# Performance work log

Hardware: AMD Instinct MI355X
Metric: run time of the kernel (lower is better)

The kernel has to match this reference:

```python
import math
import jax, jax.numpy as jnp
import numpy as np

B, W, C = 2, 2048, 1024
N, K = 16, 64  # heads, head dim (C // N)


def setup_inputs() -> dict:
    key = jax.random.key(0)
    ks = jax.random.split(key, 6)
    return {
        "in_sequence_bwc": jax.random.normal(ks[0], (B, W, C), dtype=jnp.float32),
        "W_proj": jax.random.normal(ks[1], (C, C), dtype=jnp.float32) * (1.0 / math.sqrt(C)),
        "b_proj": jax.random.normal(ks[2], (C,), dtype=jnp.float32) * 0.01,
        "generators_1nwk": jax.random.normal(ks[3], (1, N, W, K), dtype=jnp.float32),
        "W_mix": jax.random.normal(ks[4], (C, C), dtype=jnp.float32) * (1.0 / math.sqrt(C)),
        "b_mix": jax.random.normal(ks[5], (C,), dtype=jnp.float32) * 0.01,
    }


def reference(in_sequence_bwc, W_proj, b_proj, generators_1nwk, W_mix, b_mix):
    b, w, c = in_sequence_bwc.shape
    # shared projection (torch Linear: x @ W.T + b)
    p_bwc = in_sequence_bwc @ W_proj.T + b_proj
    p_bnwk = p_bwc.reshape(b, w, N, K).transpose(0, 2, 1, 3)  # [b, n, w, k]
    g_nwk = generators_1nwk[0, :, :w, :]  # [n, w, k]
    # data-dependent metric generator: p^T @ G -> [b, n, k, k]
    m_bnkk = jnp.einsum("bnwk,nwl->bnkl", p_bnwk, g_nwk)
    tril_kk = jnp.tril(jnp.ones((K, K), dtype=in_sequence_bwc.dtype))
    m_bnkk = m_bnkk * tril_kk  # lower-triangular mask on k x k
    m_bnkk = m_bnkk @ jnp.swapaxes(m_bnkk, -1, -2)  # PSD metric M M^T
    # bilinear scores: P @ M @ P^T, scaled
    pm_bnwk = jnp.einsum("bnwk,bnkl->bnwl", p_bnwk, m_bnkk)
    scores_bnww = jnp.einsum("bnwk,bnvk->bnwv", pm_bnwk, p_bnwk) / math.sqrt(K)
    causal = jnp.tril(jnp.ones((w, w), dtype=bool))
    scores_bnww = jnp.where(causal, scores_bnww, -jnp.inf)
    attn_bnww = jax.nn.softmax(scores_bnww, axis=-1)
    nudged_bnwk = attn_bnww @ p_bnwk
    nudged_bwc = nudged_bnwk.transpose(0, 2, 1, 3).reshape(b, w, c)
    return nudged_bwc @ W_mix.T + b_mix
```

## Files before the change

kernel.cpp:

```cpp
#include <hip/hip_runtime.h>
#include <math.h>

#define B_  2
#define W_  2048
#define C_  1024
#define NH_ 16
#define KD_ 64

__device__ __forceinline__ int swz2(int r, int c) {
    return (r << 6) + ((((c >> 2) ^ ((r >> 2) & 7)) << 2) | (c & 3));
}
__device__ __forceinline__ void stage_sw2(const float* __restrict__ src,
                                          float* dst, int tid, int nf4) {
    for (int idx = tid; idx < nf4; idx += 256) {
        int r = idx >> 4;
        int c = (idx & 15) << 2;
        *(float4*)&dst[swz2(r, c)] = *(const float4*)(src + (idx << 2));
    }
}

template<int OUT_P_LAYOUT>
__global__ __launch_bounds__(256, 2)
void gemm_nt(const float* __restrict__ A, const float* __restrict__ Bw,
             const float* __restrict__ bias, float* __restrict__ Cout)
{
    __shared__ float As[16][68];
    __shared__ float Bs[16][68];
    const int tid = threadIdx.x;
    const int tx  = tid & 15, ty = tid >> 4;
    const int m0  = blockIdx.x << 6;
    const int n0  = blockIdx.y << 6;
    const int lrow = tid >> 2;
    const int lkq  = (tid & 3) << 2;
    const float* Ap = A  + (size_t)(m0 + lrow) * C_ + lkq;
    const float* Bp = Bw + (size_t)(n0 + lrow) * C_ + lkq;

    float acc[4][4] = {};
    for (int k0 = 0; k0 < C_; k0 += 16) {
        float4 av = *(const float4*)(Ap + k0);
        float4 bv = *(const float4*)(Bp + k0);
        __syncthreads();
        As[lkq+0][lrow] = av.x; As[lkq+1][lrow] = av.y;
        As[lkq+2][lrow] = av.z; As[lkq+3][lrow] = av.w;
        Bs[lkq+0][lrow] = bv.x; Bs[lkq+1][lrow] = bv.y;
        Bs[lkq+2][lrow] = bv.z; Bs[lkq+3][lrow] = bv.w;
        __syncthreads();
#pragma unroll
        for (int kk = 0; kk < 16; ++kk) {
            float4 a4 = *(const float4*)&As[kk][ty << 2];
            float4 b4 = *(const float4*)&Bs[kk][tx << 2];
            float am[4] = {a4.x, a4.y, a4.z, a4.w};
            float bm[4] = {b4.x, b4.y, b4.z, b4.w};
#pragma unroll
            for (int i = 0; i < 4; ++i)
#pragma unroll
                for (int j = 0; j < 4; ++j)
                    acc[i][j] = fmaf(am[i], bm[j], acc[i][j]);
        }
    }

    const int gc = n0 + (tx << 2);
    float4 bb = *(const float4*)&bias[gc];
#pragma unroll
    for (int i = 0; i < 4; ++i) {
        int gm = m0 + (ty << 2) + i;
        float4 o;
        o.x = acc[i][0] + bb.x;
        o.y = acc[i][1] + bb.y;
        o.z = acc[i][2] + bb.z;
        o.w = acc[i][3] + bb.w;
        if (OUT_P_LAYOUT) {
            int b = gm >> 11;
            int w = gm & 2047;
            int n = gc >> 6;
            int k = gc & 63;
            *(float4*)(Cout + (((size_t)(b * NH_ + n) * W_ + w) * KD_ + k)) = o;
        } else {
            *(float4*)(Cout + (size_t)gm * C_ + gc) = o;
        }
    }
}

__global__ __launch_bounds__(256, 2)
void metric_part(const float* __restrict__ p, const float* __restrict__ g,
                 float* __restrict__ part)
{
    __shared__ float Ps[32][68];
    __shared__ float Gs[32][68];
    const int ch  = blockIdx.x;
    const int bn  = blockIdx.y;
    const int n   = bn & (NH_ - 1);
    const int tid = threadIdx.x;
    const int tx  = tid & 15, ty = tid >> 4;
    const float* pb = p + (size_t)bn * W_ * KD_ + (size_t)(ch << 8) * KD_;
    const float* gb = g + (size_t)n  * W_ * KD_ + (size_t)(ch << 8) * KD_;

    int r0[2], c0[2];
#pragma unroll
    for (int q = 0; q < 2; ++q) {
        int idx = tid + (q << 8);
        r0[q] = (idx << 2) >> 6;
        c0[q] = (idx << 2) & 63;
    }
    float4 rp[2], rg[2];
#pragma unroll
    for (int q = 0; q < 2; ++q) {
        rp[q] = *(const float4*)(pb + (size_t)r0[q] * KD_ + c0[q]);
        rg[q] = *(const float4*)(gb + (size_t)r0[q] * KD_ + c0[q]);
    }

    float acc[4][4] = {};
    for (int w0 = 0; w0 < 256; w0 += 32) {
        __syncthreads();
#pragma unroll
        for (int q = 0; q < 2; ++q) {
            *(float4*)&Ps[r0[q]][c0[q]] = rp[q];
            *(float4*)&Gs[r0[q]][c0[q]] = rg[q];
        }
        __syncthreads();
        if (w0 < 224) {
#pragma unroll
            for (int q = 0; q < 2; ++q) {
                rp[q] = *(const float4*)(pb + (size_t)(w0 + 32 + r0[q]) * KD_ + c0[q]);
                rg[q] = *(const float4*)(gb + (size_t)(w0 + 32 + r0[q]) * KD_ + c0[q]);
            }
        }
#pragma unroll 8
        for (int w = 0; w < 32; ++w) {
            float4 a4 = *(const float4*)&Ps[w][ty << 2];
            float4 b4 = *(const float4*)&Gs[w][tx << 2];
            float am[4] = {a4.x, a4.y, a4.z, a4.w};
            float bm[4] = {b4.x, b4.y, b4.z, b4.w};
#pragma unroll
            for (int i = 0; i < 4; ++i)
#pragma unroll
                for (int j = 0; j < 4; ++j)
                    acc[i][j] = fmaf(am[i], bm[j], acc[i][j]);
        }
    }

    float* ob = part + (size_t)(bn * 8 + ch) * KD_ * KD_;
#pragma unroll
    for (int i = 0; i < 4; ++i) {
        float4 o; o.x = acc[i][0]; o.y = acc[i][1]; o.z = acc[i][2]; o.w = acc[i][3];
        *(float4*)(ob + ((ty << 2) + i) * KD_ + (tx << 2)) = o;
    }
}

__global__ __launch_bounds__(256, 2)
void metric_reduce(const float* __restrict__ part, float* __restrict__ m2)
{
    __shared__ float M1s[64][68];
    const int bn  = blockIdx.x;
    const int tid = threadIdx.x;
    const int tx  = tid & 15, ty = tid >> 4;
    const float* pb = part + (size_t)bn * 8 * KD_ * KD_;

#pragma unroll
    for (int v = 0; v < 4; ++v) {
        int f = tid + (v << 8);
        int e = f << 2;
        float4 s = *(const float4*)(pb + e);
#pragma unroll
        for (int c = 1; c < 8; ++c) {
            float4 t = *(const float4*)(pb + c * 4096 + e);
            s.x += t.x; s.y += t.y; s.z += t.z; s.w += t.w;
        }
        int k = e >> 6, l = e & 63;
        if (l + 0 > k) s.x = 0.f;
        if (l + 1 > k) s.y = 0.f;
        if (l + 2 > k) s.z = 0.f;
        if (l + 3 > k) s.w = 0.f;
        *(float4*)&M1s[k][l] = s;
    }
    __syncthreads();

    float a2[4][4] = {};
#pragma unroll
    for (int jq = 0; jq < 64; jq += 4) {
        float4 av[4], bv[4];
#pragma unroll
        for (int i = 0; i < 4; ++i) av[i] = *(const float4*)&M1s[(ty << 2) + i][jq];
#pragma unroll
        for (int j = 0; j < 4; ++j) bv[j] = *(const float4*)&M1s[(tx << 2) + j][jq];
#pragma unroll
        for (int i = 0; i < 4; ++i)
#pragma unroll
            for (int j = 0; j < 4; ++j)
                a2[i][j] += av[i].x * bv[j].x + av[i].y * bv[j].y +
                            av[i].z * bv[j].z + av[i].w * bv[j].w;
    }

    float* ob = m2 + (size_t)bn * KD_ * KD_;
#pragma unroll
    for (int i = 0; i < 4; ++i) {
        float4 o; o.x = a2[i][0]; o.y = a2[i][1]; o.z = a2[i][2]; o.w = a2[i][3];
        *(float4*)(ob + ((ty << 2) + i) * KD_ + (tx << 2)) = o;
    }
}

__global__ __launch_bounds__(256, 2)
void qgen_k(const float* __restrict__ p, const float* __restrict__ m2,
            float* __restrict__ qout)
{
    __shared__ float Pt[64][68];
    __shared__ float Ms[64][68];
    const int bn  = blockIdx.y;
    const int w0  = blockIdx.x << 6;
    const int tid = threadIdx.x;
    const int tx  = tid & 15, ty = tid >> 4;
    const float* pb = p  + (size_t)bn * W_ * KD_ + (size_t)w0 * KD_;
    const float* mb = m2 + (size_t)bn * KD_ * KD_;

#pragma unroll
    for (int q = 0; q < 4; ++q) {
        int idx = tid + (q << 8);
        int e   = idx << 2;
        int r   = e >> 6;
        int c   = e & 63;
        *(float4*)&Pt[r][c] = *(const float4*)(pb + e);
        *(float4*)&Ms[r][c] = *(const float4*)(mb + e);
    }
    __syncthreads();

    float acc[4][4] = {};
#pragma unroll
    for (int kq = 0; kq < 64; kq += 4) {
        float4 av[4];
        float  bm[4][4];
#pragma unroll
        for (int i = 0; i < 4; ++i) av[i] = *(const float4*)&Pt[(ty << 2) + i][kq];
#pragma unroll
        for (int kk = 0; kk < 4; ++kk) {
            float4 t = *(const float4*)&Ms[kq + kk][tx << 2];
            bm[kk][0] = t.x; bm[kk][1] = t.y; bm[kk][2] = t.z; bm[kk][3] = t.w;
        }
#pragma unroll
        for (int i = 0; i < 4; ++i) {
            float am[4] = {av[i].x, av[i].y, av[i].z, av[i].w};
#pragma unroll
            for (int j = 0; j < 4; ++j)
                acc[i][j] = fmaf(am[0], bm[0][j],
                            fmaf(am[1], bm[1][j],
                            fmaf(am[2], bm[2][j],
                            fmaf(am[3], bm[3][j], acc[i][j]))));
        }
    }

    float* ob = qout + (size_t)bn * W_ * KD_ + (size_t)w0 * KD_;
#pragma unroll
    for (int i = 0; i < 4; ++i) {
        float4 o;
        o.x = acc[i][0] * 0.125f; o.y = acc[i][1] * 0.125f;
        o.z = acc[i][2] * 0.125f; o.w = acc[i][3] * 0.125f;
        *(float4*)(ob + ((ty << 2) + i) * KD_ + (tx << 2)) = o;
    }
}

__global__ __launch_bounds__(256, 3)
void attn_ck(const float* __restrict__ qg, const float* __restrict__ p,
             float* __restrict__ nud, float* __restrict__ part, int mode)
{
    __shared__ float Qs[4096];
    __shared__ float Ks[4096];
    __shared__ float Es[4096];
    const int bid = blockIdx.x;
    const int bn  = bid & 31;
    const int b   = bn >> 4, n = bn & 15;
    const int tid = threadIdx.x;
    const int tx  = tid & 15, ty = tid >> 4;

    int qt, js, je, direct, slot = 0;
    if (mode == 0) {
        int cid = bid >> 5;
        qt = 31 - cid; js = 0; je = qt + 1; direct = 1;
    } else {
        int cid = 59 - (bid >> 5);
        int c0;
        if (cid < 12)      { qt = cid;                c0 = 0; }
        else if (cid < 36) { qt = 12 + ((cid-12)>>1); c0 = (cid-12)&1; }
        else               { qt = 24 + (cid-36)/3;    c0 = (cid-36)%3; }
        js = c0 * 12;
        je = min(js + 12, qt + 1);
        direct = (qt < 12);
        slot = bn * 60 + cid;
    }

    const float* pb = p + (size_t)bn * W_ * KD_;
    stage_sw2(qg + (size_t)bn * W_ * KD_ + (size_t)(qt << 6) * KD_, Qs, tid, 1024);

    int sr[4], sc[4];
#pragma unroll
    for (int t = 0; t < 4; ++t) {
        int idx = tid + (t << 8);
        sr[t] = idx >> 4;
        sc[t] = (idx & 15) << 2;
    }
    float4 pk[4];
    {
        const float* kp = pb + (size_t)(js << 6) * KD_;
#pragma unroll
        for (int t = 0; t < 4; ++t)
            pk[t] = *(const float4*)(kp + ((tid + (t << 8)) << 2));
    }

    float acc[4][4] = {};
    float mi[4], li[4];
#pragma unroll
    for (int i = 0; i < 4; ++i) { mi[i] = -INFINITY; li[i] = 0.f; }

    for (int j0 = js; j0 < je; ++j0) {
        __syncthreads();
#pragma unroll
        for (int t = 0; t < 4; ++t)
            *(float4*)&Ks[swz2(sr[t], sc[t])] = pk[t];
        __syncthreads();

        if (j0 + 1 < je) {
            const float* np = pb + (size_t)((j0 + 1) << 6) * KD_;
#pragma unroll
            for (int t = 0; t < 4; ++t)
                pk[t] = *(const float4*)(np + ((tid + (t << 8)) << 2));
        }

        float s[4][4] = {};
#pragma unroll
        for (int kq = 0; kq < 64; kq += 4) {
            float4 av[4], bv[4];
#pragma unroll
            for (int i = 0; i < 4; ++i) av[i] = *(const float4*)&Qs[swz2((ty << 2) + i, kq)];
#pragma unroll
            for (int j = 0; j < 4; ++j) bv[j] = *(const float4*)&Ks[swz2((tx << 2) + j, kq)];
#pragma unroll
            for (int i = 0; i < 4; ++i)
#pragma unroll
                for (int j = 0; j < 4; ++j)
                    s[i][j] = fmaf(av[i].x, bv[j].x,
                              fmaf(av[i].y, bv[j].y,
                              fmaf(av[i].z, bv[j].z,
                              fmaf(av[i].w, bv[j].w, s[i][j]))));
        }

        if (j0 == qt) {
#pragma unroll
            for (int i = 0; i < 4; ++i)
#pragma unroll
                for (int j = 0; j < 4; ++j)
                    if (((tx << 2) + j) > ((ty << 2) + i)) s[i][j] = -INFINITY;
        }

#pragma unroll
        for (int i = 0; i < 4; ++i) {
            float rm = fmaxf(fmaxf(s[i][0], s[i][1]), fmaxf(s[i][2], s[i][3]));
            rm = fmaxf(rm, __shfl_xor(rm, 1, 16));
            rm = fmaxf(rm, __shfl_xor(rm, 2, 16));
            rm = fmaxf(rm, __shfl_xor(rm, 4, 16));
            rm = fmaxf(rm, __shfl_xor(rm, 8, 16));
            float mnew = fmaxf(mi[i], rm);
#pragma unroll
            for (int j = 0; j < 4; ++j) s[i][j] = __expf(s[i][j] - mnew);
            float rs = s[i][0] + s[i][1] + s[i][2] + s[i][3];
            rs += __shfl_xor(rs, 1, 16);
            rs += __shfl_xor(rs, 2, 16);
            rs += __shfl_xor(rs, 4, 16);
            rs += __shfl_xor(rs, 8, 16);
            float al = __expf(mi[i] - mnew);
            li[i] = li[i] * al + rs;
            mi[i] = mnew;
            float4 e; e.x = s[i][0]; e.y = s[i][1]; e.z = s[i][2]; e.w = s[i][3];
            *(float4*)&Es[swz2((ty << 2) + i, tx << 2)] = e;
#pragma unroll
            for (int j = 0; j < 4; ++j) acc[i][j] *= al;
        }
        __syncthreads();

#pragma unroll
        for (int jq = 0; jq < 64; jq += 4) {
            float4 vm[4];
#pragma unroll
            for (int kk = 0; kk < 4; ++kk) vm[kk] = *(const float4*)&Ks[swz2(jq + kk, tx << 2)];
#pragma unroll
            for (int i = 0; i < 4; ++i) {
                float4 a = *(const float4*)&Es[swz2((ty << 2) + i, jq)];
                acc[i][0] = fmaf(a.x, vm[0].x, fmaf(a.y, vm[1].x,
                            fmaf(a.z, vm[2].x, fmaf(a.w, vm[3].x, acc[i][0]))));
                acc[i][1] = fmaf(a.x, vm[0].y, fmaf(a.y, vm[1].y,
                            fmaf(a.z, vm[2].y, fmaf(a.w, vm[3].y, acc[i][1]))));
                acc[i][2] = fmaf(a.x, vm[0].z, fmaf(a.y, vm[1].z,
                            fmaf(a.z, vm[2].z, fmaf(a.w, vm[3].z, acc[i][2]))));
                acc[i][3] = fmaf(a.x, vm[0].w, fmaf(a.y, vm[1].w,
                            fmaf(a.z, vm[2].w, fmaf(a.w, vm[3].w, acc[i][3]))));
            }
        }
    }

    if (direct) {
        const int wrow = qt << 6;
#pragma unroll
        for (int i = 0; i < 4; ++i) {
            float inv = 1.f / li[i];
            float4 o;
            o.x = acc[i][0] * inv; o.y = acc[i][1] * inv;
            o.z = acc[i][2] * inv; o.w = acc[i][3] * inv;
            size_t row = (size_t)(b * W_ + wrow + (ty << 2) + i);
            *(float4*)(nud + row * C_ + (n << 6) + (tx << 2)) = o;
        }
    } else {
        float* ob = part + (size_t)slot * 4224;
#pragma unroll
        for (int i = 0; i < 4; ++i) {
            int r = (ty << 2) + i;
            float4 o;
            o.x = acc[i][0]; o.y = acc[i][1]; o.z = acc[i][2]; o.w = acc[i][3];
            *(float4*)(ob + (r << 6) + (tx << 2)) = o;
            if (tx == 0) {
                ob[4096 + r] = mi[i];
                ob[4160 + r] = li[i];
            }
        }
    }
}

__global__ __launch_bounds__(256, 2)
void combine_k(const float* __restrict__ part, float* __restrict__ nud)
{
    const int bid = blockIdx.x;
    const int bn  = bid & 31;
    const int qt  = 12 + (bid >> 5);
    const int b   = bn >> 4, n = bn & 15;
    int nc, cid0;
    if (qt < 24) { nc = 2; cid0 = 12 + ((qt - 12) << 1); }
    else         { nc = 3; cid0 = 36 + 3 * (qt - 24); }
    const float* p0 = part + (size_t)(bn * 60 + cid0) * 4224;
    const int tid = threadIdx.x;

#pragma unroll
    for (int k = 0; k < 4; ++k) {
        int f4 = tid + (k << 8);
        int e  = f4 << 2;
        int r  = e >> 6;
        float M = -INFINITY;
        for (int c = 0; c < nc; ++c)
            M = fmaxf(M, p0[c * 4224 + 4096 + r]);
        float Ox = 0.f, Oy = 0.f, Oz = 0.f, Ow = 0.f, L = 0.f;
        for (int c = 0; c < nc; ++c) {
            float w = __expf(p0[c * 4224 + 4096 + r] - M);
            float4 t = *(const float4*)(p0 + c * 4224 + e);
            Ox += w * t.x; Oy += w * t.y; Oz += w * t.z; Ow += w * t.w;
            L  += w * p0[c * 4224 + 4160 + r];
        }
        float inv = 1.f / L;
        float4 o; o.x = Ox * inv; o.y = Oy * inv; o.z = Oz * inv; o.w = Ow * inv;
        size_t row = (size_t)(b * W_ + (qt << 6) + r);
        *(float4*)(nud + row * C_ + (n << 6) + (e & 63)) = o;
    }
}

extern "C" void kernel_launch(void* const* d_in, const int* in_sizes, int n_in,
                              void* d_out, int out_size, void* d_ws, size_t ws_size,
                              hipStream_t stream)
{
    (void)in_sizes; (void)n_in; (void)out_size;
    const float* X  = (const float*)d_in[0];
    const float* Wp = (const float*)d_in[1];
    const float* bp = (const float*)d_in[2];
    const float* G  = (const float*)d_in[3];
    const float* Wm = (const float*)d_in[4];
    const float* bm = (const float*)d_in[5];
    float* out = (float*)d_out;
    float* ws  = (float*)d_ws;

    float* Pbuf  = ws;
    float* Qbuf  = ws + 4194304;
    float* M2    = ws + 8388608;
    float* Nud   = ws + 8519680;
    float* Part2 = ws + 12713984;

    const size_t needF = 12713984ULL + 1920ULL * 4224ULL;
    const bool big = ws_size >= needF * sizeof(float);
    float* MPart = big ? Part2 : Nud;

    dim3 blk(256);
    gemm_nt<1>   <<<dim3(64, 16), blk, 0, stream>>>(X, Wp, bp, Pbuf);
    metric_part  <<<dim3(8, 32),  blk, 0, stream>>>(Pbuf, G, MPart);
    metric_reduce<<<dim3(32),     blk, 0, stream>>>(MPart, M2);
    qgen_k       <<<dim3(32, 32), blk, 0, stream>>>(Pbuf, M2, Qbuf);
    if (big) {
        attn_ck  <<<dim3(1920),   blk, 0, stream>>>(Qbuf, Pbuf, Nud, Part2, 1);
        combine_k<<<dim3(640),    blk, 0, stream>>>(Part2, Nud);
    } else {
        attn_ck  <<<dim3(1024),   blk, 0, stream>>>(Qbuf, Pbuf, Nud, Part2, 0);
    }
    gemm_nt<0>   <<<dim3(64, 16), blk, 0, stream>>>(Nud, Wm, bm, out);
}
```

Baseline: 920.5 us.

## Enlarge attention query tile to 128 rows and rebalance split-K chunking

Each attention block now handles 128 query rows instead of 64, with each thread computing 8 rows. Every staged K/V tile is therefore reused across twice as many queries, halving the K/V global and LDS traffic per query. The split-KV schedule is rebuilt so query tiles are divided evenly into 1–4 chunks, and the partial buffers and combine kernel are resized to match. In exchange, LDS use roughly doubles, occupancy drops from 3 to 2 blocks per CU, register pressure rises, and the grid has fewer blocks.

```diff
diff --git a/kernel.cpp b/kernel.cpp
--- a/kernel.cpp
+++ b/kernel.cpp
@@ -6,6 +6,7 @@
 #define C_  1024
 #define NH_ 16
 #define KD_ 64
+#define PSZ 8448
 
 __device__ __forceinline__ int swz2(int r, int c) {
     return (r << 6) + ((((c >> 2) ^ ((r >> 2) & 7)) << 2) | (c & 3));
@@ -257,37 +258,41 @@
     }
 }
 
-__global__ __launch_bounds__(256, 3)
+__global__ __launch_bounds__(256, 2)
 void attn_ck(const float* __restrict__ qg, const float* __restrict__ p,
              float* __restrict__ nud, float* __restrict__ part, int mode)
 {
-    __shared__ float Qs[4096];
+    __shared__ float Qs[8192];
     __shared__ float Ks[4096];
-    __shared__ float Es[4096];
+    __shared__ float Es[8192];
     const int bid = blockIdx.x;
     const int bn  = bid & 31;
     const int b   = bn >> 4, n = bn & 15;
     const int tid = threadIdx.x;
     const int tx  = tid & 15, ty = tid >> 4;
+    const int r0  = ty << 3;
 
     int qt, js, je, direct, slot = 0;
     if (mode == 0) {
-        int cid = bid >> 5;
-        qt = 31 - cid; js = 0; je = qt + 1; direct = 1;
+        qt = 15 - (bid >> 5); js = 0; je = (qt << 1) + 2; direct = 1;
     } else {
-        int cid = 59 - (bid >> 5);
-        int c0;
-        if (cid < 12)      { qt = cid;                c0 = 0; }
-        else if (cid < 36) { qt = 12 + ((cid-12)>>1); c0 = (cid-12)&1; }
-        else               { qt = 24 + (cid-36)/3;    c0 = (cid-36)%3; }
-        js = c0 * 12;
-        je = min(js + 12, qt + 1);
-        direct = (qt < 12);
-        slot = bn * 60 + cid;
+        int cid = 39 - (bid >> 5);
+        int c, nc;
+        if (cid < 4)       { qt = cid;                c = 0;           nc = 1; }
+        else if (cid < 12) { qt = 4 + ((cid-4) >> 1); c = (cid-4) & 1; nc = 2; }
+        else if (cid < 24) { qt = 8 + (cid-12) / 3;   c = (cid-12) % 3; nc = 3; }
+        else               { qt = 12 + ((cid-24)>>2); c = (cid-24) & 3; nc = 4; }
+        int T    = (qt << 1) + 2;
+        int base = T / nc;
+        int rem  = T - base * nc;
+        js = c * base + min(c, rem);
+        je = js + base + (c < rem ? 1 : 0);
+        direct = (nc == 1);
+        slot = bn * 36 + (cid - 4);
     }
 
     const float* pb = p + (size_t)bn * W_ * KD_;
-    stage_sw2(qg + (size_t)bn * W_ * KD_ + (size_t)(qt << 6) * KD_, Qs, tid, 1024);
+    stage_sw2(qg + (size_t)bn * W_ * KD_ + (size_t)(qt << 7) * KD_, Qs, tid, 2048);
 
     int sr[4], sc[4];
 #pragma unroll
@@ -304,10 +309,10 @@
             pk[t] = *(const float4*)(kp + ((tid + (t << 8)) << 2));
     }
 
-    float acc[4][4] = {};
-    float mi[4], li[4];
-#pragma unroll
-    for (int i = 0; i < 4; ++i) { mi[i] = -INFINITY; li[i] = 0.f; }
+    float acc[8][4] = {};
+    float mi[8], li[8];
+#pragma unroll
+    for (int i = 0; i < 8; ++i) { mi[i] = -INFINITY; li[i] = 0.f; }
 
     for (int j0 = js; j0 < je; ++j0) {
         __syncthreads();
@@ -323,34 +328,33 @@
                 pk[t] = *(const float4*)(np + ((tid + (t << 8)) << 2));
         }
 
-        float s[4][4] = {};
+        float s[8][4] = {};
 #pragma unroll
         for (int kq = 0; kq < 64; kq += 4) {
-            float4 av[4], bv[4];
-#pragma unroll
-            for (int i = 0; i < 4; ++i) av[i] = *(const float4*)&Qs[swz2((ty << 2) + i, kq)];
+            float4 bv[4];
 #pragma unroll
             for (int j = 0; j < 4; ++j) bv[j] = *(const float4*)&Ks[swz2((tx << 2) + j, kq)];
 #pragma unroll
-            for (int i = 0; i < 4; ++i)
+            for (int i = 0; i < 8; ++i) {
+                float4 a = *(const float4*)&Qs[swz2(r0 + i, kq)];
 #pragma unroll
                 for (int j = 0; j < 4; ++j)
-                    s[i][j] = fmaf(av[i].x, bv[j].x,
-                              fmaf(av[i].y, bv[j].y,
-                              fmaf(av[i].z, bv[j].z,
-                              fmaf(av[i].w, bv[j].w, s[i][j]))));
-        }
-
-        if (j0 == qt) {
-#pragma unroll
-            for (int i = 0; i < 4; ++i)
+                    s[i][j] = fmaf(a.x, bv[j].x, fmaf(a.y, bv[j].y,
+                              fmaf(a.z, bv[j].z, fmaf(a.w, bv[j].w, s[i][j]))));
+            }
+        }
+
+        if (j0 >= (qt << 1)) {
+            int cb = ((j0 - (qt << 1)) << 6) + (tx << 2);
+#pragma unroll
+            for (int i = 0; i < 8; ++i)
 #pragma unroll
                 for (int j = 0; j < 4; ++j)
-                    if (((tx << 2) + j) > ((ty << 2) + i)) s[i][j] = -INFINITY;
-        }
-
-#pragma unroll
-        for (int i = 0; i < 4; ++i) {
+                    if (cb + j > r0 + i) s[i][j] = -INFINITY;
+        }
+
+#pragma unroll
+        for (int i = 0; i < 8; ++i) {
             float rm = fmaxf(fmaxf(s[i][0], s[i][1]), fmaxf(s[i][2], s[i][3]));
             rm = fmaxf(rm, __shfl_xor(rm, 1, 16));
             rm = fmaxf(rm, __shfl_xor(rm, 2, 16));
@@ -368,7 +372,7 @@
             li[i] = li[i] * al + rs;
             mi[i] = mnew;
             float4 e; e.x = s[i][0]; e.y = s[i][1]; e.z = s[i][2]; e.w = s[i][3];
-            *(float4*)&Es[swz2((ty << 2) + i, tx << 2)] = e;
+            *(float4*)&Es[swz2(r0 + i, tx << 2)] = e;
 #pragma unroll
             for (int j = 0; j < 4; ++j) acc[i][j] *= al;
         }
@@ -380,8 +384,8 @@
 #pragma unroll
             for (int kk = 0; kk < 4; ++kk) vm[kk] = *(const float4*)&Ks[swz2(jq + kk, tx << 2)];
 #pragma unroll
-            for (int i = 0; i < 4; ++i) {
-                float4 a = *(const float4*)&Es[swz2((ty << 2) + i, jq)];
+            for (int i = 0; i < 8; ++i) {
+                float4 a = *(const float4*)&Es[swz2(r0 + i, jq)];
                 acc[i][0] = fmaf(a.x, vm[0].x, fmaf(a.y, vm[1].x,
                             fmaf(a.z, vm[2].x, fmaf(a.w, vm[3].x, acc[i][0]))));
                 acc[i][1] = fmaf(a.x, vm[0].y, fmaf(a.y, vm[1].y,
@@ -395,27 +399,27 @@
     }
 
     if (direct) {
-        const int wrow = qt << 6;
-#pragma unroll
-        for (int i = 0; i < 4; ++i) {
+        const int wrow = qt << 7;
+#pragma unroll
+        for (int i = 0; i < 8; ++i) {
             float inv = 1.f / li[i];
             float4 o;
             o.x = acc[i][0] * inv; o.y = acc[i][1] * inv;
             o.z = acc[i][2] * inv; o.w = acc[i][3] * inv;
-            size_t row = (size_t)(b * W_ + wrow + (ty << 2) + i);
+            size_t row = (size_t)(b * W_ + wrow + r0 + i);
             *(float4*)(nud + row * C_ + (n << 6) + (tx << 2)) = o;
         }
     } else {
-        float* ob = part + (size_t)slot * 4224;
-#pragma unroll
-        for (int i = 0; i < 4; ++i) {
-            int r = (ty << 2) + i;
+        float* ob = part + (size_t)slot * PSZ;
+#pragma unroll
+        for (int i = 0; i < 8; ++i) {
+            int r = r0 + i;
             float4 o;
             o.x = acc[i][0]; o.y = acc[i][1]; o.z = acc[i][2]; o.w = acc[i][3];
             *(float4*)(ob + (r << 6) + (tx << 2)) = o;
             if (tx == 0) {
-                ob[4096 + r] = mi[i];
-                ob[4160 + r] = li[i];
+                ob[8192 + r] = mi[i];
+                ob[8320 + r] = li[i];
             }
         }
     }
@@ -426,32 +430,34 @@
 {
     const int bid = blockIdx.x;
     const int bn  = bid & 31;
-    const int qt  = 12 + (bid >> 5);
+    const int qt  = 4 + (bid >> 5);
     const int b   = bn >> 4, n = bn & 15;
-    int nc, cid0;
-    if (qt < 24) { nc = 2; cid0 = 12 + ((qt - 12) << 1); }
-    else         { nc = 3; cid0 = 36 + 3 * (qt - 24); }
-    const float* p0 = part + (size_t)(bn * 60 + cid0) * 4224;
+    const int nc  = (qt >> 2) + 1;
+    int cid0;
+    if (qt < 8)       cid0 = 4  + ((qt - 4)  << 1);
+    else if (qt < 12) cid0 = 12 + (qt - 8) * 3;
+    else              cid0 = 24 + ((qt - 12) << 2);
+    const float* p0 = part + (size_t)(bn * 36 + cid0 - 4) * PSZ;
     const int tid = threadIdx.x;
 
 #pragma unroll
-    for (int k = 0; k < 4; ++k) {
+    for (int k = 0; k < 8; ++k) {
         int f4 = tid + (k << 8);
         int e  = f4 << 2;
         int r  = e >> 6;
         float M = -INFINITY;
         for (int c = 0; c < nc; ++c)
-            M = fmaxf(M, p0[c * 4224 + 4096 + r]);
+            M = fmaxf(M, p0[c * PSZ + 8192 + r]);
         float Ox = 0.f, Oy = 0.f, Oz = 0.f, Ow = 0.f, L = 0.f;
         for (int c = 0; c < nc; ++c) {
-            float w = __expf(p0[c * 4224 + 4096 + r] - M);
-            float4 t = *(const float4*)(p0 + c * 4224 + e);
+            float w = __expf(p0[c * PSZ + 8192 + r] - M);
+            float4 t = *(const float4*)(p0 + c * PSZ + e);
             Ox += w * t.x; Oy += w * t.y; Oz += w * t.z; Ow += w * t.w;
-            L  += w * p0[c * 4224 + 4160 + r];
+            L  += w * p0[c * PSZ + 8320 + r];
         }
         float inv = 1.f / L;
         float4 o; o.x = Ox * inv; o.y = Oy * inv; o.z = Oz * inv; o.w = Ow * inv;
-        size_t row = (size_t)(b * W_ + (qt << 6) + r);
+        size_t row = (size_t)(b * W_ + (qt << 7) + r);
         *(float4*)(nud + row * C_ + (n << 6) + (e & 63)) = o;
     }
 }
@@ -476,7 +482,7 @@
     float* Nud   = ws + 8519680;
     float* Part2 = ws + 12713984;
 
-    const size_t needF = 12713984ULL + 1920ULL * 4224ULL;
+    const size_t needF = 12713984ULL + 32ULL * 36ULL * PSZ;
     const bool big = ws_size >= needF * sizeof(float);
     float* MPart = big ? Part2 : Nud;
 
@@ -486,10 +492,10 @@
     metric_reduce<<<dim3(32),     blk, 0, stream>>>(MPart, M2);
     qgen_k       <<<dim3(32, 32), blk, 0, stream>>>(Pbuf, M2, Qbuf);
     if (big) {
-        attn_ck  <<<dim3(1920),   blk, 0, stream>>>(Qbuf, Pbuf, Nud, Part2, 1);
-        combine_k<<<dim3(640),    blk, 0, stream>>>(Part2, Nud);
+        attn_ck  <<<dim3(1280),   blk, 0, stream>>>(Qbuf, Pbuf, Nud, Part2, 1);
+        combine_k<<<dim3(384),    blk, 0, stream>>>(Part2, Nud);
     } else {
-        attn_ck  <<<dim3(1024),   blk, 0, stream>>>(Qbuf, Pbuf, Nud, Part2, 0);
+        attn_ck  <<<dim3(512),    blk, 0, stream>>>(Qbuf, Pbuf, Nud, Part2, 0);
     }
     gemm_nt<0>   <<<dim3(64, 16), blk, 0, stream>>>(Nud, Wm, bm, out);
 }
```

Measured after the change: 1.072 ms. 16.5% more time.
